# Kernel optimization log

Hardware: AMD Instinct MI355X
Metric: run time of the kernel (lower is better)

## Reference

```python
import jax, jax.numpy as jnp
import numpy as np

N = 8192
E = 262144
IN_F = 128
OUT_F = 128


def setup_inputs() -> dict:
    key = jax.random.key(0)
    k1, k2, k3, k4 = jax.random.split(key, 4)
    x = jax.random.normal(k1, (N, IN_F), dtype=jnp.float32)
    adj = jax.random.randint(k2, (2, E), 0, N, dtype=jnp.int64)
    edge_w = jax.random.uniform(k3, (E,), dtype=jnp.float32)
    # Kaiming-normal-style init for weight (std = sqrt(2/fan_in)); zero bias.
    weight = jax.random.normal(k4, (IN_F, OUT_F), dtype=jnp.float32) * np.sqrt(2.0 / IN_F)
    bias = jnp.zeros((OUT_F,), dtype=jnp.float32)
    return {"x": x, "adj": adj, "edge_w": edge_w, "weight": weight, "bias": bias}


def reference(x, adj, edge_w, weight, bias):
    eps = 1e-10
    n = x.shape[0]
    support = x @ weight  # [N, out_features]
    # Densify COO adjacency (duplicate indices sum, matching sparse_coo_tensor.to_dense)
    adj_dense = jnp.zeros((n, n), dtype=x.dtype).at[adj[0], adj[1]].add(edge_w)
    adj_dense = adj_dense + jnp.eye(n, dtype=x.dtype)  # add self-loops
    deg = jnp.sum(adj_dense, axis=1)  # [N]
    d_inv_sqrt = 1.0 / jnp.sqrt(deg + eps)
    # D^{-1/2} A D^{-1/2} expressed as row/col scaling (same math as diag matmuls)
    norm_adj = d_inv_sqrt[:, None] * adj_dense * d_inv_sqrt[None, :]
    # include_bias=True path
    return norm_adj @ support + bias
```

## Files before the change

### kernel.cpp

```cpp
#include <hip/hip_runtime.h>
#include <math.h>

#define N_NODES 8192
#define NE      262144
#define F       128
#define CAP     96
#define NBLK    64
#define CAP_B   16
#define GBLKS   256

#define FMA4(acc, xs, wq) \
    acc.x += (xs) * (wq).x; acc.y += (xs) * (wq).y; acc.z += (xs) * (wq).z; acc.w += (xs) * (wq).w;

__global__ __launch_bounds__(256) void k_fused(const float* __restrict__ x,
                                               const int* __restrict__ adj,
                                               const float* __restrict__ ew,
                                               const float* __restrict__ wmat,
                                               int* __restrict__ cnt_out,
                                               int2* __restrict__ slots,
                                               float* __restrict__ support) {
    __shared__ union {
        int cnt[N_NODES];
        struct { float xT[128][68]; float wl[128][68]; } g;
    } sh;
    int tid = threadIdx.x;

    if (blockIdx.x < NBLK) {
        int blk = blockIdx.x;
#pragma unroll
        for (int j = 0; j < 8; j++)
            *(int4*)&sh.cnt[tid * 4 + j * 1024] = make_int4(0, 0, 0, 0);
        __syncthreads();

        int base_e = blk * 4096 + tid * 16;
#pragma unroll
        for (int ch = 0; ch < 4; ch++) {
            int e0 = base_e + ch * 4;
            int4   rr = *(const int4*)(adj + e0);
            int4   cc = *(const int4*)(adj + NE + e0);
            float4 wv = *(const float4*)(ew + e0);
            int r[4] = {rr.x, rr.y, rr.z, rr.w};
            int c[4] = {cc.x, cc.y, cc.z, cc.w};
            float wl4[4] = {wv.x, wv.y, wv.z, wv.w};
            int pos[4];
#pragma unroll
            for (int j = 0; j < 4; j++)
                pos[j] = atomicAdd(&sh.cnt[r[j]], 1);
#pragma unroll
            for (int j = 0; j < 4; j++)
                if (pos[j] < CAP_B)
                    slots[((size_t)blk * N_NODES + r[j]) * CAP_B + pos[j]] =
                        make_int2(c[j], __float_as_int(wl4[j]));
        }
        __syncthreads();
#pragma unroll
        for (int j = 0; j < 8; j++)
            *(int4*)&cnt_out[(size_t)blk * N_NODES + tid * 4 + j * 1024] =
                *(int4*)&sh.cnt[tid * 4 + j * 1024];
        return;
    }

    int g   = blockIdx.x - NBLK;
    int R0  = (g >> 1) * 64;
    int chf = g & 1;
    {
        int row = tid & 63;
        int w0  = tid >> 6;
        const float* xr = x + (size_t)(R0 + row) * F;
#pragma unroll
        for (int j = 0; j < 8; j++) {
            int c0 = w0 * 4 + 16 * j;
            float4 v = *(const float4*)(xr + c0);
            sh.g.xT[c0 + 0][row] = v.x;
            sh.g.xT[c0 + 1][row] = v.y;
            sh.g.xT[c0 + 2][row] = v.z;
            sh.g.xT[c0 + 3][row] = v.w;
        }
    }
    {
#pragma unroll
        for (int j = 0; j < 8; j++) {
            int q  = tid + 256 * j;
            int k  = q & 127;
            int c0 = 4 * (q >> 7);
            float4 v = *(const float4*)(wmat + (size_t)k * F + chf * 64 + c0);
            *(float4*)&sh.g.wl[k][c0] = v;
        }
    }
    __syncthreads();

    if (tid >= 128) return;

    int w  = tid >> 6;
    int l  = tid & 63;
    int r0 = (l >> 3) * 8;
    int c0 = w * 32 + (l & 7) * 4;

    float4 a0 = {0,0,0,0}, a1 = {0,0,0,0}, a2 = {0,0,0,0}, a3 = {0,0,0,0};
    float4 a4 = {0,0,0,0}, a5 = {0,0,0,0}, a6 = {0,0,0,0}, a7 = {0,0,0,0};
#pragma unroll 4
    for (int k = 0; k < F; k++) {
        float4 xv0 = *(const float4*)&sh.g.xT[k][r0];
        float4 xv1 = *(const float4*)&sh.g.xT[k][r0 + 4];
        float4 wq  = *(const float4*)&sh.g.wl[k][c0];
        FMA4(a0, xv0.x, wq); FMA4(a1, xv0.y, wq); FMA4(a2, xv0.z, wq); FMA4(a3, xv0.w, wq);
        FMA4(a4, xv1.x, wq); FMA4(a5, xv1.y, wq); FMA4(a6, xv1.z, wq); FMA4(a7, xv1.w, wq);
    }
    float* sp = support + (size_t)(R0 + r0) * F + chf * 64 + c0;
    *(float4*)(sp + 0 * F) = a0;  *(float4*)(sp + 1 * F) = a1;
    *(float4*)(sp + 2 * F) = a2;  *(float4*)(sp + 3 * F) = a3;
    *(float4*)(sp + 4 * F) = a4;  *(float4*)(sp + 5 * F) = a5;
    *(float4*)(sp + 6 * F) = a6;  *(float4*)(sp + 7 * F) = a7;
}

__global__ __launch_bounds__(256) void k_merge(const int* __restrict__ cnt_out,
                                               const int2* __restrict__ slots,
                                               int* __restrict__ cnt_dense,
                                               int2* __restrict__ dense,
                                               float* __restrict__ deg) {
    __shared__ int   cnts[NBLK][32];
    __shared__ int   pref[NBLK][32];
    __shared__ float wsum[32];
    __shared__ int   tot[32];
    int tid = threadIdx.x;
    int r0  = blockIdx.x * 32;

    if (tid < 32) wsum[tid] = 0.f;
#pragma unroll
    for (int p = 0; p < 8; p++) {
        int blk = p * 8 + (tid >> 5);
        int row = tid & 31;
        int cc = cnt_out[(size_t)blk * N_NODES + r0 + row];
        if (cc > CAP_B) cc = CAP_B;
        cnts[blk][row] = cc;
    }
    __syncthreads();
    if (tid < 32) {
        int run = 0;
#pragma unroll 8
        for (int k = 0; k < NBLK; k++) {
            pref[k][tid] = run;
            run += cnts[k][tid];
        }
        tot[tid] = run;
    }
    __syncthreads();
#pragma unroll
    for (int j = 0; j < 8; j++) {
        int cell = j * 256 + tid;
        int blk  = cell >> 5;
        int row  = cell & 31;
        int n    = cnts[blk][row];
        if (n == 0) continue;
        int base = pref[blk][row];
        const int2* src = slots + ((size_t)blk * N_NODES + r0 + row) * CAP_B;
        int2* dst = dense + (size_t)(r0 + row) * CAP;
        float ws = 0.f;
        for (int k = 0; k < n; k++) {
            int2 e = src[k];
            ws += __int_as_float(e.y);
            if (base + k < CAP) dst[base + k] = e;
        }
        atomicAdd(&wsum[row], ws);
    }
    __syncthreads();
    if (tid < 32) {
        deg[r0 + tid] = wsum[tid];
        int t = tot[tid];
        cnt_dense[r0 + tid] = t < CAP ? t : CAP;
    }
}

__global__ __launch_bounds__(256) void k_spmm(const float* __restrict__ support,
                                              const float* __restrict__ deg,
                                              const int* __restrict__ cnt_dense,
                                              const int2* __restrict__ dense,
                                              const float* __restrict__ bias,
                                              float* __restrict__ out) {
    int l = threadIdx.x & 63;
    int i = blockIdx.x * 4 + (threadIdx.x >> 6);
    int f = l * 2;
    float2 bv = *(const float2*)(bias + f);
    float di = rsqrtf(deg[i] + 1.0f + 1e-10f);
    int cnt = cnt_dense[i];
    const int2* row = dense + (size_t)i * CAP;
    float2 a0 = *(const float2*)(support + (size_t)i * F + f);
    a0.x *= di; a0.y *= di;
    float2 a1 = {0.f, 0.f}, a2 = {0.f, 0.f}, a3 = {0.f, 0.f};
    int j = 0;
    for (; j + 4 <= cnt; j += 4) {
        int2 p0 = row[j + 0];
        int2 p1 = row[j + 1];
        int2 p2 = row[j + 2];
        int2 p3 = row[j + 3];
        float c0 = __int_as_float(p0.y) * rsqrtf(deg[p0.x] + 1.0f + 1e-10f);
        float c1 = __int_as_float(p1.y) * rsqrtf(deg[p1.x] + 1.0f + 1e-10f);
        float c2 = __int_as_float(p2.y) * rsqrtf(deg[p2.x] + 1.0f + 1e-10f);
        float c3 = __int_as_float(p3.y) * rsqrtf(deg[p3.x] + 1.0f + 1e-10f);
        float2 s0 = *(const float2*)(support + (size_t)p0.x * F + f);
        float2 s1 = *(const float2*)(support + (size_t)p1.x * F + f);
        float2 s2 = *(const float2*)(support + (size_t)p2.x * F + f);
        float2 s3 = *(const float2*)(support + (size_t)p3.x * F + f);
        a0.x += c0 * s0.x; a0.y += c0 * s0.y;
        a1.x += c1 * s1.x; a1.y += c1 * s1.y;
        a2.x += c2 * s2.x; a2.y += c2 * s2.y;
        a3.x += c3 * s3.x; a3.y += c3 * s3.y;
    }
    for (; j < cnt; j++) {
        int2 p = row[j];
        float cc = __int_as_float(p.y) * rsqrtf(deg[p.x] + 1.0f + 1e-10f);
        float2 sv = *(const float2*)(support + (size_t)p.x * F + f);
        a0.x += cc * sv.x; a0.y += cc * sv.y;
    }
    float2 r;
    r.x = di * ((a0.x + a1.x) + (a2.x + a3.x)) + bv.x;
    r.y = di * ((a0.y + a1.y) + (a2.y + a3.y)) + bv.y;
    *(float2*)(out + (size_t)i * F + f) = r;
}

extern "C" void kernel_launch(void* const* d_in, const int* in_sizes, int n_in,
                              void* d_out, int out_size, void* d_ws, size_t ws_size,
                              hipStream_t stream) {
    const float* x    = (const float*)d_in[0];
    const int*   adj  = (const int*)d_in[1];
    const float* ew   = (const float*)d_in[2];
    const float* w    = (const float*)d_in[3];
    const float* bias = (const float*)d_in[4];
    float* out = (float*)d_out;

    char*  ws        = (char*)d_ws;
    float* support   = (float*)(ws);
    float* deg       = (float*)(ws + (4u << 20));
    int*   cnt_dense = (int*)  (ws + (4u << 20) + 32768);
    int2*  dense     = (int2*) (ws + (4u << 20) + 65536);
    int*   cnt_out   = (int*)  (ws + (11u << 20));
    int2*  slots     = (int2*) (ws + (13u << 20));

    k_fused<<<NBLK + GBLKS, 256, 0, stream>>>(x, adj, ew, w, cnt_out, slots, support);
    k_merge<<<N_NODES / 32, 256, 0, stream>>>(cnt_out, slots, cnt_dense, dense, deg);
    k_spmm<<<N_NODES / 4, 256, 0, stream>>>(support, deg, cnt_dense, dense, bias, out);
}
```

Measured before the change: 111.3 us.

## Replace per-block fixed-capacity row slots with compact shared-memory counting-sort bins

After: 115.2 us. 1.03x slower.

```diff
diff --git a/kernel.cpp b/kernel.cpp
--- a/kernel.cpp
+++ b/kernel.cpp
@@ -6,7 +6,7 @@
 #define F       128
 #define CAP     96
 #define NBLK    64
-#define CAP_B   16
+#define EPB     4096
 #define GBLKS   256
 
 #define FMA4(acc, xs, wq) \
@@ -16,11 +16,11 @@
                                                const int* __restrict__ adj,
                                                const float* __restrict__ ew,
                                                const float* __restrict__ wmat,
-                                               int* __restrict__ cnt_out,
-                                               int2* __restrict__ slots,
+                                               int* __restrict__ start_out,
+                                               int2* __restrict__ bins,
                                                float* __restrict__ support) {
     __shared__ union {
-        int cnt[N_NODES];
+        struct { int cnt[N_NODES]; int2 bin[EPB]; int part[256]; } e;
         struct { float xT[128][68]; float wl[128][68]; } g;
     } sh;
     int tid = threadIdx.x;
@@ -29,34 +29,61 @@
         int blk = blockIdx.x;
 #pragma unroll
         for (int j = 0; j < 8; j++)
-            *(int4*)&sh.cnt[tid * 4 + j * 1024] = make_int4(0, 0, 0, 0);
-        __syncthreads();
-
-        int base_e = blk * 4096 + tid * 16;
+            *(int4*)&sh.e.cnt[tid * 4 + j * 1024] = make_int4(0, 0, 0, 0);
+        __syncthreads();
+
+        int base_e = blk * EPB + tid * 16;
+        int4 r4[4];
+#pragma unroll
+        for (int ch = 0; ch < 4; ch++) r4[ch] = *(const int4*)(adj + base_e + ch * 4);
+#pragma unroll
+        for (int ch = 0; ch < 4; ch++) {
+            atomicAdd(&sh.e.cnt[r4[ch].x], 1);
+            atomicAdd(&sh.e.cnt[r4[ch].y], 1);
+            atomicAdd(&sh.e.cnt[r4[ch].z], 1);
+            atomicAdd(&sh.e.cnt[r4[ch].w], 1);
+        }
+        __syncthreads();
+
+        int loc[32];
+        int run = 0;
+#pragma unroll
+        for (int k = 0; k < 32; k++) { loc[k] = run; run += sh.e.cnt[tid * 32 + k]; }
+        sh.e.part[tid] = run;
+        __syncthreads();
+        for (int off = 1; off < 256; off <<= 1) {
+            int v = (tid >= off) ? sh.e.part[tid - off] : 0;
+            __syncthreads();
+            sh.e.part[tid] += v;
+            __syncthreads();
+        }
+        int base0 = sh.e.part[tid] - run;
+        __syncthreads();
+#pragma unroll
+        for (int k = 0; k < 32; k++) sh.e.cnt[tid * 32 + k] = base0 + loc[k];
+        __syncthreads();
+#pragma unroll
+        for (int j = 0; j < 8; j++)
+            *(int4*)&start_out[(size_t)blk * N_NODES + tid * 4 + j * 1024] =
+                *(int4*)&sh.e.cnt[tid * 4 + j * 1024];
+        __syncthreads();
+
 #pragma unroll
         for (int ch = 0; ch < 4; ch++) {
             int e0 = base_e + ch * 4;
-            int4   rr = *(const int4*)(adj + e0);
             int4   cc = *(const int4*)(adj + NE + e0);
             float4 wv = *(const float4*)(ew + e0);
-            int r[4] = {rr.x, rr.y, rr.z, rr.w};
-            int c[4] = {cc.x, cc.y, cc.z, cc.w};
-            float wl4[4] = {wv.x, wv.y, wv.z, wv.w};
-            int pos[4];
-#pragma unroll
-            for (int j = 0; j < 4; j++)
-                pos[j] = atomicAdd(&sh.cnt[r[j]], 1);
-#pragma unroll
-            for (int j = 0; j < 4; j++)
-                if (pos[j] < CAP_B)
-                    slots[((size_t)blk * N_NODES + r[j]) * CAP_B + pos[j]] =
-                        make_int2(c[j], __float_as_int(wl4[j]));
+            int pos;
+            pos = atomicAdd(&sh.e.cnt[r4[ch].x], 1); sh.e.bin[pos] = make_int2(cc.x, __float_as_int(wv.x));
+            pos = atomicAdd(&sh.e.cnt[r4[ch].y], 1); sh.e.bin[pos] = make_int2(cc.y, __float_as_int(wv.y));
+            pos = atomicAdd(&sh.e.cnt[r4[ch].z], 1); sh.e.bin[pos] = make_int2(cc.z, __float_as_int(wv.z));
+            pos = atomicAdd(&sh.e.cnt[r4[ch].w], 1); sh.e.bin[pos] = make_int2(cc.w, __float_as_int(wv.w));
         }
         __syncthreads();
 #pragma unroll
         for (int j = 0; j < 8; j++)
-            *(int4*)&cnt_out[(size_t)blk * N_NODES + tid * 4 + j * 1024] =
-                *(int4*)&sh.cnt[tid * 4 + j * 1024];
+            ((int4*)bins)[(size_t)blk * 2048 + tid + j * 256] =
+                ((int4*)sh.e.bin)[tid + j * 256];
         return;
     }
 
@@ -113,11 +140,12 @@
     *(float4*)(sp + 6 * F) = a6;  *(float4*)(sp + 7 * F) = a7;
 }
 
-__global__ __launch_bounds__(256) void k_merge(const int* __restrict__ cnt_out,
-                                               const int2* __restrict__ slots,
+__global__ __launch_bounds__(256) void k_merge(const int* __restrict__ start_out,
+                                               const int2* __restrict__ bins,
                                                int* __restrict__ cnt_dense,
                                                int2* __restrict__ dense,
                                                float* __restrict__ deg) {
+    __shared__ int   starts_l[NBLK][32];
     __shared__ int   cnts[NBLK][32];
     __shared__ int   pref[NBLK][32];
     __shared__ float wsum[32];
@@ -130,18 +158,17 @@
     for (int p = 0; p < 8; p++) {
         int blk = p * 8 + (tid >> 5);
         int row = tid & 31;
-        int cc = cnt_out[(size_t)blk * N_NODES + r0 + row];
-        if (cc > CAP_B) cc = CAP_B;
-        cnts[blk][row] = cc;
+        int gr  = r0 + row;
+        int s = start_out[(size_t)blk * N_NODES + gr];
+        int e = (gr == N_NODES - 1) ? EPB : start_out[(size_t)blk * N_NODES + gr + 1];
+        starts_l[blk][row] = s;
+        cnts[blk][row] = e - s;
     }
     __syncthreads();
     if (tid < 32) {
         int run = 0;
 #pragma unroll 8
-        for (int k = 0; k < NBLK; k++) {
-            pref[k][tid] = run;
-            run += cnts[k][tid];
-        }
+        for (int k = 0; k < NBLK; k++) { pref[k][tid] = run; run += cnts[k][tid]; }
         tot[tid] = run;
     }
     __syncthreads();
@@ -152,8 +179,9 @@
         int row  = cell & 31;
         int n    = cnts[blk][row];
         if (n == 0) continue;
+        int s    = starts_l[blk][row];
         int base = pref[blk][row];
-        const int2* src = slots + ((size_t)blk * N_NODES + r0 + row) * CAP_B;
+        const int2* src = bins + (size_t)blk * EPB + s;
         int2* dst = dense + (size_t)(r0 + row) * CAP;
         float ws = 0.f;
         for (int k = 0; k < n; k++) {
@@ -233,10 +261,10 @@
     float* deg       = (float*)(ws + (4u << 20));
     int*   cnt_dense = (int*)  (ws + (4u << 20) + 32768);
     int2*  dense     = (int2*) (ws + (4u << 20) + 65536);
-    int*   cnt_out   = (int*)  (ws + (11u << 20));
-    int2*  slots     = (int2*) (ws + (13u << 20));
-
-    k_fused<<<NBLK + GBLKS, 256, 0, stream>>>(x, adj, ew, w, cnt_out, slots, support);
-    k_merge<<<N_NODES / 32, 256, 0, stream>>>(cnt_out, slots, cnt_dense, dense, deg);
+    int*   start_out = (int*)  (ws + (11u << 20));
+    int2*  bins      = (int2*) (ws + (13u << 20));
+
+    k_fused<<<NBLK + GBLKS, 256, 0, stream>>>(x, adj, ew, w, start_out, bins, support);
+    k_merge<<<N_NODES / 32, 256, 0, stream>>>(start_out, bins, cnt_dense, dense, deg);
     k_spmm<<<N_NODES / 4, 256, 0, stream>>>(support, deg, cnt_dense, dense, bias, out);
 }
```
